# Kernel tuning notes

Measured on AMD Instinct MI355X. Metric: run time of the kernel, lower is better.

The kernel has to match this reference:

```python
import jax, jax.numpy as jnp
import numpy as np

TOP_K = 2

def setup_inputs() -> dict:
    key = jax.random.key(0)
    ks = jax.random.split(key, 5)
    B, S, D, E, R, H = 4, 2048, 1024, 8, 128, 4096
    s = 0.02
    return {
        "hidden_states": jax.random.normal(ks[0], (B, S, D), jnp.float32),
        "w_route": jax.random.normal(ks[1], (E, D, R), jnp.float32) * s,
        "w3": jax.random.normal(ks[2], (E, D, H), jnp.float32) * s,
        "wr2h": jax.random.normal(ks[3], (E, R, H), jnp.float32) * s,
        "wh2d": jax.random.normal(ks[4], (E, H, D), jnp.float32) * s,
    }

def reference(hidden_states, w_route, w3, wr2h, wh2d):
    B, S, D = hidden_states.shape
    E = w_route.shape[0]
    x = hidden_states.reshape(-1, D)                      # [N, D]
    N = x.shape[0]
    # per-expert routing activations (also reused as w1_state inside experts)
    acts = jnp.einsum('nd,edr->ner', x, w_route)          # [N, E, R]
    norms = jnp.linalg.norm(acts, axis=-1)                # [N, E] router logits
    probs = jax.nn.softmax(norms.astype(jnp.float32), axis=-1)
    topw, sel = jax.lax.top_k(probs, TOP_K)               # [N, k]
    topw = topw / topw.sum(axis=-1, keepdims=True)
    topw = topw.astype(x.dtype)
    # dense combine weights: routing weight if expert selected, else 0
    combine = jnp.zeros((N, E), x.dtype).at[jnp.arange(N)[:, None], sel].add(topw)
    out = jnp.zeros_like(x)
    for e in range(E):  # fixed small expert count
        h = (x @ w3[e]) * jax.nn.silu(acts[:, e, :] @ wr2h[e])  # [N, H]
        out = out + (h @ wh2d[e]) * combine[:, e:e + 1]
    final = out.reshape(B, S, D)
    # load balancing loss on the router logits (expert_act_norms)
    mask = jax.nn.one_hot(sel, E, dtype=jnp.float32)      # [N, k, E]
    tokens_per_expert = mask.mean(axis=0)                 # [k, E]
    router_prob_per_expert = probs.mean(axis=0)           # [E]
    bl_loss = jnp.sum(tokens_per_expert * router_prob_per_expert[None, :]) * E
    return final, norms, bl_loss
```

## Files before the change

### kernel.cpp

```cpp
#include <hip/hip_runtime.h>


#define DEV static __device__ __forceinline__

typedef float  f32x4  __attribute__((ext_vector_type(4)));
typedef __bf16 bf16x8 __attribute__((ext_vector_type(8)));

DEV unsigned short f2bf(float f) {
  union { float f; unsigned u; } v; v.f = f;
  unsigned r = v.u + 0x7fffu + ((v.u >> 16) & 1u);
  return (unsigned short)(r >> 16);
}
DEV float bf2f(unsigned short b) {
  union { unsigned u; float f; } v; v.u = ((unsigned)b) << 16;
  return v.f;
}

DEV void gll16(const void* g, void* l) {
  __builtin_amdgcn_global_load_lds(
      (const __attribute__((address_space(1))) unsigned int*)g,
      (__attribute__((address_space(3))) unsigned int*)l, 16, 0, 0);
}

DEV f32x4 mfma16(bf16x8 a, bf16x8 b, f32x4 c) {
  return __builtin_amdgcn_mfma_f32_16x16x32_bf16(a, b, c, 0, 0, 0);
}

DEV int xcd_swz(int bid, int nwg) {
  int q = nwg >> 3;
  return (bid & 7) * q + (bid >> 3);
}

DEV void stage_linear(const unsigned short* base, size_t pitch, int k0,
                      unsigned short* lds, int tid) {
  int wq = tid >> 6, lane = tid & 63;
#pragma unroll
  for (int i = 0; i < 4; ++i) {
    int s = wq * 256 + i * 64 + lane;
    int row = s >> 3, b = s & 7;
    int bb = b ^ (row & 7);
    const unsigned short* g = base + (size_t)row * pitch + (size_t)(k0 + bb * 8);
    gll16(g, lds + (size_t)(wq * 256 + i * 64) * 8);
  }
}

DEV void stage_gather(const unsigned short* base, size_t pitch, size_t colOff,
                      int k0, const int* toks, unsigned short* lds, int tid) {
  int wq = tid >> 6, lane = tid & 63;
#pragma unroll
  for (int i = 0; i < 4; ++i) {
    int s = wq * 256 + i * 64 + lane;
    int row = s >> 3, b = s & 7;
    int bb = b ^ (row & 7);
    const unsigned short* g =
        base + (size_t)toks[row] * pitch + colOff + (size_t)(k0 + bb * 8);
    gll16(g, lds + (size_t)(wq * 256 + i * 64) * 8);
  }
}

DEV bf16x8 frag_read(const unsigned short* lds, int row, int kb) {
  int off = row * 128 + ((kb * 2) ^ ((row & 7) << 4));
  return *(const bf16x8*)((const char*)lds + off);
}

DEV void mfma_block(const unsigned short* A, const unsigned short* B,
                    f32x4 (&acc)[4][4], int wm, int wn, int lg, int lc) {
#pragma unroll
  for (int ks = 0; ks < 2; ++ks) {
    int kb = ks * 32 + lg * 8;
    bf16x8 af[4], bff[4];
#pragma unroll
    for (int i = 0; i < 4; ++i) {
      af[i]  = frag_read(A, wm * 64 + i * 16 + lc, kb);
      bff[i] = frag_read(B, wn * 64 + i * 16 + lc, kb);
    }
#pragma unroll
    for (int mf = 0; mf < 4; ++mf)
#pragma unroll
      for (int nf = 0; nf < 4; ++nf)
        acc[mf][nf] = mfma16(af[mf], bff[nf], acc[mf][nf]);
  }
}


__global__ __launch_bounds__(256) void k_cast_x(const float* __restrict__ x,
    unsigned short* __restrict__ xh, unsigned short* __restrict__ xl) {
  int stride = gridDim.x * blockDim.x;
  for (int i = blockIdx.x * blockDim.x + threadIdx.x; i < 8192 * 1024 / 4;
       i += stride) {
    float4 v = ((const float4*)x)[i];
    ushort4 h, l;
    h.x = f2bf(v.x); l.x = f2bf(v.x - bf2f(h.x));
    h.y = f2bf(v.y); l.y = f2bf(v.y - bf2f(h.y));
    h.z = f2bf(v.z); l.z = f2bf(v.z - bf2f(h.z));
    h.w = f2bf(v.w); l.w = f2bf(v.w - bf2f(h.w));
    ((ushort4*)xh)[i] = h;
    ((ushort4*)xl)[i] = l;
  }
}

__global__ void k_zero(int* cnt, float* probsum) {
  int t = threadIdx.x;
  if (t < 16) cnt[t] = 0;
  if (t < 8)  probsum[t] = 0.f;
}

__global__ __launch_bounds__(256) void k_transp(const float* __restrict__ src,
    unsigned short* __restrict__ dst, int K, int N) {
  int ntn = N >> 6;
  int kt = blockIdx.x / ntn, nt = blockIdx.x % ntn;
  int e = blockIdx.y;
  __shared__ float tl[64][65];
  const float* s = src + (size_t)e * K * N;
  unsigned short* d = dst + (size_t)e * N * K;
  int tid = threadIdx.x;
  int c4 = (tid & 15) * 4, rr = tid >> 4;
#pragma unroll
  for (int p = 0; p < 4; ++p) {
    int row = rr + p * 16;
    float4 v = *(const float4*)(s + (size_t)(kt * 64 + row) * N + nt * 64 + c4);
    tl[row][c4] = v.x; tl[row][c4 + 1] = v.y;
    tl[row][c4 + 2] = v.z; tl[row][c4 + 3] = v.w;
  }
  __syncthreads();
#pragma unroll
  for (int p = 0; p < 4; ++p) {
    int n = rr + p * 16;
    ushort4 o;
    o.x = f2bf(tl[c4 + 0][n]); o.y = f2bf(tl[c4 + 1][n]);
    o.z = f2bf(tl[c4 + 2][n]); o.w = f2bf(tl[c4 + 3][n]);
    *(ushort4*)(d + (size_t)(nt * 64 + n) * K + kt * 64 + c4) = o;
  }
// ... 102 lines not shown
    for (int r = 0; r < 4; ++r) {
      float s = ssq[mf][r];
      s += __shfl_xor(s, 1); s += __shfl_xor(s, 2);
      s += __shfl_xor(s, 4); s += __shfl_xor(s, 8);
      if (lc == 0) ssq_s[wm * 64 + mf * 16 + lg * 4 + r][wn] = s;
    }
  __syncthreads();
  if (tid < 128) {
    float s = ssq_s[tid][0] + ssq_s[tid][1];
    norms_out[(size_t)(mt * 128 + tid) * 8 + e] = sqrtf(s);
  }
}

__global__ __launch_bounds__(256) void k_router(const float* __restrict__ norms,
    float* __restrict__ topw, int* __restrict__ sel,
    int* __restrict__ cnt, float* __restrict__ probsum) {
  __shared__ float ps_s[8];
  __shared__ int cnt_s[16];
  int tid = threadIdx.x;
  if (tid < 8)  ps_s[tid] = 0.f;
  if (tid < 16) cnt_s[tid] = 0;
  __syncthreads();
  int n = blockIdx.x * 256 + tid;
  float p[8], mx = -3.4e38f;
#pragma unroll
  for (int e = 0; e < 8; ++e) { p[e] = norms[(size_t)n * 8 + e]; mx = fmaxf(mx, p[e]); }
  float s = 0.f;
#pragma unroll
  for (int e = 0; e < 8; ++e) { p[e] = __expf(p[e] - mx); s += p[e]; }
  float inv = 1.f / s;
  int i1 = 0; float v1 = p[0];
#pragma unroll
  for (int e = 1; e < 8; ++e) if (p[e] > v1) { v1 = p[e]; i1 = e; }
  int i2 = -1; float v2 = -1.f;
#pragma unroll
  for (int e = 0; e < 8; ++e) if (e != i1 && p[e] > v2) { v2 = p[e]; i2 = e; }
  float wsum = v1 + v2;
  topw[n * 2 + 0] = v1 / wsum;
  topw[n * 2 + 1] = v2 / wsum;
  sel[n * 2 + 0] = i1;
  sel[n * 2 + 1] = i2;
  atomicAdd(&cnt_s[i1], 1);
  atomicAdd(&cnt_s[8 + i2], 1);
#pragma unroll
  for (int e = 0; e < 8; ++e) atomicAdd(&ps_s[e], p[e] * inv);
  __syncthreads();
  if (tid < 8)  atomicAdd(&probsum[tid], ps_s[tid]);
  if (tid < 16) atomicAdd(&cnt[tid], cnt_s[tid]);
}

__global__ void k_plan(const int* __restrict__ cnt, const float* __restrict__ probsum,
                       int* __restrict__ offs, int* __restrict__ fill,
                       int4* __restrict__ tilemap, float* __restrict__ bl_out) {
  int t = 0;
  for (int k = 0; k < 2; ++k) {
    int pos = 0;
    for (int e = 0; e < 8; ++e) {
      int c = cnt[k * 8 + e];
      offs[k * 8 + e] = pos;
      int ntl = (c + 127) >> 7;
      for (int i = 0; i < ntl; ++i) {
        int rr = c - i * 128; if (rr > 128) rr = 128;
        tilemap[t] = make_int4(e, k * 8192 + pos + i * 128, rr, 0);
        ++t;
      }
      pos += c;
    }
  }
  for (; t < 144; ++t) tilemap[t] = make_int4(0, 0, 0, 0);
  for (int i = 0; i < 16; ++i) fill[i] = 0;
  float bl = 0.f;
  for (int e = 0; e < 8; ++e)
    bl += ((float)(cnt[e] + cnt[8 + e]) / 8192.f) * (probsum[e] / 8192.f);
  *bl_out = bl * 8.f;
}

__global__ __launch_bounds__(256) void k_fill(const int* __restrict__ sel,
    const float* __restrict__ topw, const int* __restrict__ offs,
    int* __restrict__ fill, int* __restrict__ list01, float* __restrict__ wlist) {
  int n = blockIdx.x * 256 + threadIdx.x;
#pragma unroll
  for (int k = 0; k < 2; ++k) {
    int e = sel[n * 2 + k];
    int pos = atomicAdd(&fill[k * 8 + e], 1);
    int idx = k * 8192 + offs[k * 8 + e] + pos;
    list01[idx] = n;
    wlist[idx] = topw[n * 2 + k];
  }
}

__global__ __launch_bounds__(256) void k_gemm1(
    const unsigned short* __restrict__ xh, const unsigned short* __restrict__ acts,
    const unsigned short* __restrict__ w3t, const unsigned short* __restrict__ wr2h_t,
    const int* __restrict__ list, const int4* __restrict__ tilemap, int tile_lo,
    int nt, unsigned short* __restrict__ hbuf) {
  __shared__ __align__(16) unsigned short SA[2 * 128 * 64];
  __shared__ __align__(16) unsigned short SB[2 * 128 * 64];
  __shared__ int toks[128];
  int wg = xcd_swz(blockIdx.x, nt * 32);
  int tileIdx = wg >> 5, bn = wg & 31;
  int4 ent = tilemap[tile_lo + tileIdx];
  int e = ent.x, posbase = ent.y, rows = ent.z;
  if (rows == 0) return;
  int tid = threadIdx.x;
  if (tid < 128) {
    int rr = tid < rows ? tid : rows - 1;
    toks[tid] = list[posbase + rr];
  }
  __syncthreads();
  int wq = tid >> 6, lane = tid & 63;
  int wm = wq >> 1, wn = wq & 1, lg = lane >> 4, lc = lane & 15;
  f32x4 acc_a[4][4] = {};
  const unsigned short* bsrc = w3t + ((size_t)e * 4096 + bn * 128) * 1024;
  stage_gather(xh, 1024, 0, 0, toks, SA, tid);
  stage_linear(bsrc, 1024, 0, SB, tid);
  __syncthreads();
  int cur = 0;
  for (int kt = 0; kt < 15; ++kt) {
    int nxt = cur ^ 1;
    stage_gather(xh, 1024, 0, (kt + 1) * 64, toks, SA + nxt * 8192, tid);
    stage_linear(bsrc, 1024, (kt + 1) * 64, SB + nxt * 8192, tid);
    mfma_block(SA + cur * 8192, SB + cur * 8192, acc_a, wm, wn, lg, lc);
    __syncthreads();
    cur = nxt;
  }
  mfma_block(SA + cur * 8192, SB + cur * 8192, acc_a, wm, wn, lg, lc);
  __syncthreads();
  f32x4 acc_s[4][4] = {};
  const unsigned short* b2src = wr2h_t + ((size_t)e * 4096 + bn * 128) * 128;
  stage_gather(acts, 1024, (size_t)e * 128, 0, toks, SA, tid);
  stage_linear(b2src, 128, 0, SB, tid);
  stage_gather(acts, 1024, (size_t)e * 128, 64, toks, SA + 8192, tid);
  stage_linear(b2src, 128, 64, SB + 8192, tid);
  __syncthreads();
  mfma_block(SA, SB, acc_s, wm, wn, lg, lc);
  mfma_block(SA + 8192, SB + 8192, acc_s, wm, wn, lg, lc);
  size_t hrow0 = (size_t)tileIdx * 128;
#pragma unroll
  for (int mf = 0; mf < 4; ++mf)
#pragma unroll
    for (int nf = 0; nf < 4; ++nf)
#pragma unroll
      for (int r = 0; r < 4; ++r) {
        int row = wm * 64 + mf * 16 + lg * 4 + r;
        if (row < rows) {
          int col = wn * 64 + nf * 16 + lc;
          float sv = acc_s[mf][nf][r];
          float hv = acc_a[mf][nf][r] * (sv / (1.f + __expf(-sv)));
          hbuf[(hrow0 + row) * 4096 + (size_t)bn * 128 + col] = f2bf(hv);
        }
      }
}

__global__ __launch_bounds__(256) void k_gemm2(
    const unsigned short* __restrict__ hbuf, const unsigned short* __restrict__ wh2dt,
    const int* __restrict__ list, const float* __restrict__ wlist,
    const int4* __restrict__ tilemap, int tile_lo, int nt,
    float* __restrict__ out) {
  __shared__ __align__(16) unsigned short SA[2 * 128 * 64];
  __shared__ __align__(16) unsigned short SB[2 * 128 * 64];
  __shared__ int toks[128];
  __shared__ float wr_s[128];
  int wg = xcd_swz(blockIdx.x, nt * 8);
  int tileIdx = wg >> 3, bn = wg & 7;
  int4 ent = tilemap[tile_lo + tileIdx];
  int e = ent.x, posbase = ent.y, rows = ent.z;
  if (rows == 0) return;
  int tid = threadIdx.x;
  if (tid < 128) {
    int rr = tid < rows ? tid : rows - 1;
    toks[tid] = list[posbase + rr];
    wr_s[tid] = wlist[posbase + rr];
  }
  __syncthreads();
  int wq = tid >> 6, lane = tid & 63;
  int wm = wq >> 1, wn = wq & 1, lg = lane >> 4, lc = lane & 15;
  f32x4 acc[4][4] = {};
  const unsigned short* asrc = hbuf + (size_t)tileIdx * 128 * 4096;
  const unsigned short* bsrc = wh2dt + ((size_t)e * 1024 + bn * 128) * 4096;
  stage_linear(asrc, 4096, 0, SA, tid);
  stage_linear(bsrc, 4096, 0, SB, tid);
  __syncthreads();
  int cur = 0;
  for (int kt = 0; kt < 63; ++kt) {
    int nxt = cur ^ 1;
    stage_linear(asrc, 4096, (kt + 1) * 64, SA + nxt * 8192, tid);
    stage_linear(bsrc, 4096, (kt + 1) * 64, SB + nxt * 8192, tid);
    mfma_block(SA + cur * 8192, SB + cur * 8192, acc, wm, wn, lg, lc);
    __syncthreads();
    cur = nxt;
  }
  mfma_block(SA + cur * 8192, SB + cur * 8192, acc, wm, wn, lg, lc);
#pragma unroll
  for (int mf = 0; mf < 4; ++mf)
#pragma unroll
    for (int nf = 0; nf < 4; ++nf)
#pragma unroll
      for (int r = 0; r < 4; ++r) {
        int row = wm * 64 + mf * 16 + lg * 4 + r;
        if (row < rows) {
          int col = wn * 64 + nf * 16 + lc;
          float v = acc[mf][nf][r] * wr_s[row];
          atomicAdd(out + (size_t)toks[row] * 1024 + bn * 128 + col, v);
        }
      }
}


extern "C" void kernel_launch(void* const* d_in, const int* in_sizes, int n_in,
                              void* d_out, int out_size, void* d_ws, size_t ws_size,
                              hipStream_t stream) {
  (void)in_sizes; (void)n_in; (void)out_size;
  const float* x      = (const float*)d_in[0];
  const float* wroute = (const float*)d_in[1];
  const float* w3     = (const float*)d_in[2];
  const float* wr2h   = (const float*)d_in[3];
  const float* wh2d   = (const float*)d_in[4];
  float* out = (float*)d_out;

  char* ws = (char*)d_ws;
  size_t off = 0;
  auto carve = [&](size_t bytes) -> void* {
    void* p = ws + off; off += (bytes + 255) & ~(size_t)255; return p;
  };
  unsigned short* xh     = (unsigned short*)carve((size_t)8192 * 1024 * 2);
  unsigned short* xl     = (unsigned short*)carve((size_t)8192 * 1024 * 2);
  unsigned short* wrh_t  = (unsigned short*)carve((size_t)8 * 128 * 1024 * 2);
  unsigned short* wrl_t  = (unsigned short*)carve((size_t)8 * 128 * 1024 * 2);
  unsigned short* w3t    = (unsigned short*)carve((size_t)8 * 4096 * 1024 * 2);
  unsigned short* wr2h_t = (unsigned short*)carve((size_t)8 * 4096 * 128 * 2);
  unsigned short* wh2dt  = (unsigned short*)carve((size_t)8 * 1024 * 4096 * 2);
  unsigned short* acts   = (unsigned short*)carve((size_t)8192 * 1024 * 2);
  int*   list01 = (int*)carve(2 * 8192 * 4);
  float* wlist  = (float*)carve(2 * 8192 * 4);
  int*   sel    = (int*)carve(8192 * 2 * 4);
  float* topw   = (float*)carve(8192 * 2 * 4);
  int*   ctr    = (int*)carve(8192);
  int* cnt = ctr; int* fill = ctr + 16; int* offs = ctr + 32;
  float* probsum = (float*)(ctr + 48);
  int4* tilemap = (int4*)(ctr + 64);

  size_t avail = ws_size > off ? ws_size - off : 0;
  int tpc = 0;
  const int cands[8] = {144, 72, 48, 36, 24, 18, 12, 9};
  for (int i = 0; i < 8; ++i) {
    if ((size_t)cands[i] * 128 * 4096 * 2 <= avail) { tpc = cands[i]; break; }
  }
  if (!tpc) return;
  unsigned short* hbuf = (unsigned short*)(ws + off);

  float* norms_out = out + 8388608;
  float* bl_out    = out + 8454144;

  hipMemsetAsync(out, 0, (size_t)8388608 * 4, stream);
  k_cast_x<<<2048, 256, 0, stream>>>(x, xh, xl);
  k_zero<<<1, 64, 0, stream>>>(cnt, probsum);
  k_transp<<<dim3(16 * 64, 8), 256, 0, stream>>>(w3, w3t, 1024, 4096);
  k_transp<<<dim3(64 * 16, 8), 256, 0, stream>>>(wh2d, wh2dt, 4096, 1024);
  k_transp<<<dim3(2 * 64, 8), 256, 0, stream>>>(wr2h, wr2h_t, 128, 4096);
  k_transp_split<<<dim3(16 * 2, 8), 256, 0, stream>>>(wroute, wrh_t, wrl_t, 1024, 128);
  k_route_gemm<<<dim3(64, 8), 256, 0, stream>>>(xh, xl, wrh_t, wrl_t, acts, norms_out);
  k_router<<<32, 256, 0, stream>>>(norms_out, topw, sel, cnt, probsum);
  k_plan<<<1, 1, 0, stream>>>(cnt, probsum, offs, fill, tilemap, bl_out);
  k_fill<<<32, 256, 0, stream>>>(sel, topw, offs, fill, list01, wlist);

  int nchunk = (144 + tpc - 1) / tpc;
  for (int c = 0; c < nchunk; ++c) {
    int tile_lo = c * tpc;
    int nt = 144 - tile_lo < tpc ? 144 - tile_lo : tpc;
    k_gemm1<<<nt * 32, 256, 0, stream>>>(
        xh, acts, w3t, wr2h_t, list01, tilemap, tile_lo, nt, hbuf);
    k_gemm2<<<nt * 8, 256, 0, stream>>>(
        hbuf, wh2dt, list01, wlist, tilemap, tile_lo, nt, out);
  }
}
```

Before: 889.9 us.

## Enlarge expert GEMM tiles to 256 rows with 512-thread workgroups

Grouped expert GEMMs now use 256-token tiles instead of 128. gemm1 uses 256x128 tiles over 8 waves and prefetches the wr2h stage into the double buffer. gemm2 uses 256x256 tiles, which halves the weight reloads per token and the number of output atomics per element. The planner now emits at most 80 tiles and uses a generalized XCD swizzle for grid sizes not divisible by 8. Larger tiles add more padding waste on partially filled expert tiles, and the bigger LDS footprint (128KB in gemm2) may limit occupancy.

```diff
diff --git a/kernel.cpp b/kernel.cpp
--- a/kernel.cpp
+++ b/kernel.cpp
@@ -26,9 +26,15 @@
   return __builtin_amdgcn_mfma_f32_16x16x32_bf16(a, b, c, 0, 0, 0);
 }
 
-DEV int xcd_swz(int bid, int nwg) {
-  int q = nwg >> 3;
-  return (bid & 7) * q + (bid >> 3);
+DEV int xcd_swz_gen(int bid, int nwg) {
+  int x = bid & 7, o = bid >> 3;
+  int q = nwg >> 3, r = nwg & 7;
+  return (x < r ? x * (q + 1) : r * (q + 1) + (x - r) * q) + o;
+}
+
+DEV bf16x8 frag_read(const unsigned short* lds, int row, int kb) {
+  int off = row * 128 + ((kb * 2) ^ ((row & 7) << 4));
+  return *(const bf16x8*)((const char*)lds + off);
 }
 
 DEV void stage_linear(const unsigned short* base, size_t pitch, int k0,
@@ -44,23 +50,44 @@
   }
 }
 
-DEV void stage_gather(const unsigned short* base, size_t pitch, size_t colOff,
-                      int k0, const int* toks, unsigned short* lds, int tid) {
+DEV void stage_l256(const unsigned short* base, size_t pitch, int k0,
+                    unsigned short* lds, int tid) {
   int wq = tid >> 6, lane = tid & 63;
 #pragma unroll
   for (int i = 0; i < 4; ++i) {
-    int s = wq * 256 + i * 64 + lane;
+    int sb = wq * 256 + i * 64;
+    int s = sb + lane;
     int row = s >> 3, b = s & 7;
     int bb = b ^ (row & 7);
-    const unsigned short* g =
-        base + (size_t)toks[row] * pitch + colOff + (size_t)(k0 + bb * 8);
-    gll16(g, lds + (size_t)(wq * 256 + i * 64) * 8);
-  }
-}
-
-DEV bf16x8 frag_read(const unsigned short* lds, int row, int kb) {
-  int off = row * 128 + ((kb * 2) ^ ((row & 7) << 4));
-  return *(const bf16x8*)((const char*)lds + off);
+    gll16(base + (size_t)row * pitch + (size_t)(k0 + bb * 8),
+          lds + (size_t)sb * 8);
+  }
+}
+DEV void stage_g256(const unsigned short* base, size_t pitch, size_t colOff,
+                    int k0, const int* toks, unsigned short* lds, int tid) {
+  int wq = tid >> 6, lane = tid & 63;
+#pragma unroll
+  for (int i = 0; i < 4; ++i) {
+    int sb = wq * 256 + i * 64;
+    int s = sb + lane;
+    int row = s >> 3, b = s & 7;
+    int bb = b ^ (row & 7);
+    gll16(base + (size_t)toks[row] * pitch + colOff + (size_t)(k0 + bb * 8),
+          lds + (size_t)sb * 8);
+  }
+}
+DEV void stage_l128(const unsigned short* base, size_t pitch, int k0,
+                    unsigned short* lds, int tid) {
+  int wq = tid >> 6, lane = tid & 63;
+#pragma unroll
+  for (int i = 0; i < 2; ++i) {
+    int sb = wq * 128 + i * 64;
+    int s = sb + lane;
+    int row = s >> 3, b = s & 7;
+    int bb = b ^ (row & 7);
+    gll16(base + (size_t)row * pitch + (size_t)(k0 + bb * 8),
+          lds + (size_t)sb * 8);
+  }
 }
 
 DEV void mfma_block(const unsigned short* A, const unsigned short* B,
@@ -78,6 +105,40 @@
     for (int mf = 0; mf < 4; ++mf)
 #pragma unroll
       for (int nf = 0; nf < 4; ++nf)
+        acc[mf][nf] = mfma16(af[mf], bff[nf], acc[mf][nf]);
+  }
+}
+DEV void mfma256x256(const unsigned short* A, const unsigned short* B,
+                     f32x4 (&acc)[8][4], int wm, int wn, int lg, int lc) {
+#pragma unroll
+  for (int ks = 0; ks < 2; ++ks) {
+    int kb = ks * 32 + lg * 8;
+    bf16x8 af[8], bff[4];
+#pragma unroll
+    for (int i = 0; i < 8; ++i) af[i] = frag_read(A, wm * 128 + i * 16 + lc, kb);
+#pragma unroll
+    for (int i = 0; i < 4; ++i) bff[i] = frag_read(B, wn * 64 + i * 16 + lc, kb);
+#pragma unroll
+    for (int mf = 0; mf < 8; ++mf)
+#pragma unroll
+      for (int nf = 0; nf < 4; ++nf)
+        acc[mf][nf] = mfma16(af[mf], bff[nf], acc[mf][nf]);
+  }
+}
+DEV void mfma256x128(const unsigned short* A, const unsigned short* B,
+                     f32x4 (&acc)[8][2], int wm, int wn, int lg, int lc) {
+#pragma unroll
+  for (int ks = 0; ks < 2; ++ks) {
+    int kb = ks * 32 + lg * 8;
+    bf16x8 af[8], bff[2];
+#pragma unroll
+    for (int i = 0; i < 8; ++i) af[i] = frag_read(A, wm * 128 + i * 16 + lc, kb);
+#pragma unroll
+    for (int i = 0; i < 2; ++i) bff[i] = frag_read(B, wn * 32 + i * 16 + lc, kb);
+#pragma unroll
+    for (int mf = 0; mf < 8; ++mf)
+#pragma unroll
+      for (int nf = 0; nf < 2; ++nf)
         acc[mf][nf] = mfma16(af[mf], bff[nf], acc[mf][nf]);
   }
 }
@@ -292,16 +353,16 @@
     for (int e = 0; e < 8; ++e) {
       int c = cnt[k * 8 + e];
       offs[k * 8 + e] = pos;
-      int ntl = (c + 127) >> 7;
+      int ntl = (c + 255) >> 8;
       for (int i = 0; i < ntl; ++i) {
-        int rr = c - i * 128; if (rr > 128) rr = 128;
-        tilemap[t] = make_int4(e, k * 8192 + pos + i * 128, rr, 0);
+        int rr = c - i * 256; if (rr > 256) rr = 256;
+        tilemap[t] = make_int4(e, k * 8192 + pos + i * 256, rr, 0);
         ++t;
       }
       pos += c;
     }
   }
-  for (; t < 144; ++t) tilemap[t] = make_int4(0, 0, 0, 0);
+  for (; t < 80; ++t) tilemap[t] = make_int4(0, 0, 0, 0);
   for (int i = 0; i < 16; ++i) fill[i] = 0;
   float bl = 0.f;
   for (int e = 0; e < 8; ++e)
@@ -323,62 +384,62 @@
   }
 }
 
-__global__ __launch_bounds__(256) void k_gemm1(
+__global__ __launch_bounds__(512, 2) void k_gemm1(
     const unsigned short* __restrict__ xh, const unsigned short* __restrict__ acts,
     const unsigned short* __restrict__ w3t, const unsigned short* __restrict__ wr2h_t,
     const int* __restrict__ list, const int4* __restrict__ tilemap, int tile_lo,
     int nt, unsigned short* __restrict__ hbuf) {
-  __shared__ __align__(16) unsigned short SA[2 * 128 * 64];
-  __shared__ __align__(16) unsigned short SB[2 * 128 * 64];
-  __shared__ int toks[128];
-  int wg = xcd_swz(blockIdx.x, nt * 32);
-  int tileIdx = wg >> 5, bn = wg & 31;
-  int4 ent = tilemap[tile_lo + tileIdx];
+  __shared__ __align__(16) unsigned short SA[2][256 * 64];
+  __shared__ __align__(16) unsigned short SB[2][128 * 64];
+  __shared__ int toks[256];
+  int wg = xcd_swz_gen((int)blockIdx.x, nt * 32);
+  int tloc = wg >> 5, bn = wg & 31;
+  int4 ent = tilemap[tile_lo + tloc];
   int e = ent.x, posbase = ent.y, rows = ent.z;
   if (rows == 0) return;
   int tid = threadIdx.x;
-  if (tid < 128) {
+  if (tid < 256) {
     int rr = tid < rows ? tid : rows - 1;
     toks[tid] = list[posbase + rr];
   }
   __syncthreads();
   int wq = tid >> 6, lane = tid & 63;
-  int wm = wq >> 1, wn = wq & 1, lg = lane >> 4, lc = lane & 15;
-  f32x4 acc_a[4][4] = {};
-  const unsigned short* bsrc = w3t + ((size_t)e * 4096 + bn * 128) * 1024;
-  stage_gather(xh, 1024, 0, 0, toks, SA, tid);
-  stage_linear(bsrc, 1024, 0, SB, tid);
+  int wm = wq >> 2, wn = wq & 3, lg = lane >> 4, lc = lane & 15;
+  f32x4 acc_a[8][2] = {}, acc_s[8][2] = {};
+  const unsigned short* bsrc  = w3t + ((size_t)e * 4096 + bn * 128) * 1024;
+  const unsigned short* b2src = wr2h_t + ((size_t)e * 4096 + bn * 128) * 128;
+  stage_g256(xh, 1024, 0, 0, toks, SA[0], tid);
+  stage_l128(bsrc, 1024, 0, SB[0], tid);
   __syncthreads();
   int cur = 0;
   for (int kt = 0; kt < 15; ++kt) {
-    int nxt = cur ^ 1;
-    stage_gather(xh, 1024, 0, (kt + 1) * 64, toks, SA + nxt * 8192, tid);
-    stage_linear(bsrc, 1024, (kt + 1) * 64, SB + nxt * 8192, tid);
-    mfma_block(SA + cur * 8192, SB + cur * 8192, acc_a, wm, wn, lg, lc);
+    stage_g256(xh, 1024, 0, (kt + 1) * 64, toks, SA[cur ^ 1], tid);
+    stage_l128(bsrc, 1024, (kt + 1) * 64, SB[cur ^ 1], tid);
+    mfma256x128(SA[cur], SB[cur], acc_a, wm, wn, lg, lc);
     __syncthreads();
-    cur = nxt;
-  }
-  mfma_block(SA + cur * 8192, SB + cur * 8192, acc_a, wm, wn, lg, lc);
-  __syncthreads();
-  f32x4 acc_s[4][4] = {};
-  const unsigned short* b2src = wr2h_t + ((size_t)e * 4096 + bn * 128) * 128;
-  stage_gather(acts, 1024, (size_t)e * 128, 0, toks, SA, tid);
-  stage_linear(b2src, 128, 0, SB, tid);
-  stage_gather(acts, 1024, (size_t)e * 128, 64, toks, SA + 8192, tid);
-  stage_linear(b2src, 128, 64, SB + 8192, tid);
-  __syncthreads();
-  mfma_block(SA, SB, acc_s, wm, wn, lg, lc);
-  mfma_block(SA + 8192, SB + 8192, acc_s, wm, wn, lg, lc);
-  size_t hrow0 = (size_t)tileIdx * 128;
-#pragma unroll
-  for (int mf = 0; mf < 4; ++mf)
-#pragma unroll
-    for (int nf = 0; nf < 4; ++nf)
+    cur ^= 1;
+  }
+  stage_g256(acts, 1024, (size_t)e * 128, 0, toks, SA[cur ^ 1], tid);
+  stage_l128(b2src, 128, 0, SB[cur ^ 1], tid);
+  mfma256x128(SA[cur], SB[cur], acc_a, wm, wn, lg, lc);
+  __syncthreads();
+  cur ^= 1;
+  stage_g256(acts, 1024, (size_t)e * 128, 64, toks, SA[cur ^ 1], tid);
+  stage_l128(b2src, 128, 64, SB[cur ^ 1], tid);
+  mfma256x128(SA[cur], SB[cur], acc_s, wm, wn, lg, lc);
+  __syncthreads();
+  cur ^= 1;
+  mfma256x128(SA[cur], SB[cur], acc_s, wm, wn, lg, lc);
+  size_t hrow0 = (size_t)tloc * 256;
+#pragma unroll
+  for (int mf = 0; mf < 8; ++mf)
+#pragma unroll
+    for (int nf = 0; nf < 2; ++nf)
 #pragma unroll
       for (int r = 0; r < 4; ++r) {
-        int row = wm * 64 + mf * 16 + lg * 4 + r;
+        int row = wm * 128 + mf * 16 + lg * 4 + r;
         if (row < rows) {
-          int col = wn * 64 + nf * 16 + lc;
+          int col = wn * 32 + nf * 16 + lc;
           float sv = acc_s[mf][nf][r];
           float hv = acc_a[mf][nf][r] * (sv / (1.f + __expf(-sv)));
           hbuf[(hrow0 + row) * 4096 + (size_t)bn * 128 + col] = f2bf(hv);
@@ -386,56 +447,56 @@
       }
 }
 
-__global__ __launch_bounds__(256) void k_gemm2(
+__global__ __launch_bounds__(512, 2) void k_gemm2(
     const unsigned short* __restrict__ hbuf, const unsigned short* __restrict__ wh2dt,
     const int* __restrict__ list, const float* __restrict__ wlist,
     const int4* __restrict__ tilemap, int tile_lo, int nt,
     float* __restrict__ out) {
-  __shared__ __align__(16) unsigned short SA[2 * 128 * 64];
-  __shared__ __align__(16) unsigned short SB[2 * 128 * 64];
-  __shared__ int toks[128];
-  __shared__ float wr_s[128];
-  int wg = xcd_swz(blockIdx.x, nt * 8);
-  int tileIdx = wg >> 3, bn = wg & 7;
-  int4 ent = tilemap[tile_lo + tileIdx];
+  __shared__ __align__(16) unsigned short SA[2][256 * 64];
+  __shared__ __align__(16) unsigned short SB[2][256 * 64];
+  __shared__ int toks[256];
+  __shared__ float wr_s[256];
+  int wg = xcd_swz_gen((int)blockIdx.x, nt * 4);
+  int tloc = wg >> 2, bn = wg & 3;
+  int4 ent = tilemap[tile_lo + tloc];
   int e = ent.x, posbase = ent.y, rows = ent.z;
   if (rows == 0) return;
   int tid = threadIdx.x;
-  if (tid < 128) {
+  if (tid < 256) {
     int rr = tid < rows ? tid : rows - 1;
-    toks[tid] = list[posbase + rr];
+    int t = list[posbase + rr];
+    toks[tid] = t;
     wr_s[tid] = wlist[posbase + rr];
   }
   __syncthreads();
   int wq = tid >> 6, lane = tid & 63;
-  int wm = wq >> 1, wn = wq & 1, lg = lane >> 4, lc = lane & 15;
-  f32x4 acc[4][4] = {};
-  const unsigned short* asrc = hbuf + (size_t)tileIdx * 128 * 4096;
-  const unsigned short* bsrc = wh2dt + ((size_t)e * 1024 + bn * 128) * 4096;
-  stage_linear(asrc, 4096, 0, SA, tid);
-  stage_linear(bsrc, 4096, 0, SB, tid);
+  int wm = wq >> 2, wn = wq & 3, lg = lane >> 4, lc = lane & 15;
+  f32x4 acc[8][4] = {};
+  const unsigned short* asrc = hbuf + (size_t)tloc * 256 * 4096;
+  const unsigned short* bsrc = wh2dt + ((size_t)e * 1024 + bn * 256) * 4096;
+  stage_l256(asrc, 4096, 0, SA[0], tid);
+  stage_l256(bsrc, 4096, 0, SB[0], tid);
   __syncthreads();
   int cur = 0;
   for (int kt = 0; kt < 63; ++kt) {
-    int nxt = cur ^ 1;
-    stage_linear(asrc, 4096, (kt + 1) * 64, SA + nxt * 8192, tid);
-    stage_linear(bsrc, 4096, (kt + 1) * 64, SB + nxt * 8192, tid);
-    mfma_block(SA + cur * 8192, SB + cur * 8192, acc, wm, wn, lg, lc);
+    stage_l256(asrc, 4096, (kt + 1) * 64, SA[cur ^ 1], tid);
+    stage_l256(bsrc, 4096, (kt + 1) * 64, SB[cur ^ 1], tid);
+    mfma256x256(SA[cur], SB[cur], acc, wm, wn, lg, lc);
     __syncthreads();
-    cur = nxt;
-  }
-  mfma_block(SA + cur * 8192, SB + cur * 8192, acc, wm, wn, lg, lc);
-#pragma unroll
-  for (int mf = 0; mf < 4; ++mf)
+    cur ^= 1;
+  }
+  mfma256x256(SA[cur], SB[cur], acc, wm, wn, lg, lc);
+#pragma unroll
+  for (int mf = 0; mf < 8; ++mf)
 #pragma unroll
     for (int nf = 0; nf < 4; ++nf)
 #pragma unroll
       for (int r = 0; r < 4; ++r) {
-        int row = wm * 64 + mf * 16 + lg * 4 + r;
+        int row = wm * 128 + mf * 16 + lg * 4 + r;
         if (row < rows) {
           int col = wn * 64 + nf * 16 + lc;
           float v = acc[mf][nf][r] * wr_s[row];
-          atomicAdd(out + (size_t)toks[row] * 1024 + bn * 128 + col, v);
+          atomicAdd(out + (size_t)toks[row] * 1024 + bn * 256 + col, v);
         }
       }
 }
@@ -476,9 +537,9 @@
 
   size_t avail = ws_size > off ? ws_size - off : 0;
   int tpc = 0;
-  const int cands[8] = {144, 72, 48, 36, 24, 18, 12, 9};
-  for (int i = 0; i < 8; ++i) {
-    if ((size_t)cands[i] * 128 * 4096 * 2 <= avail) { tpc = cands[i]; break; }
+  const int cands[4] = {80, 40, 20, 10};
+  for (int i = 0; i < 4; ++i) {
+    if ((size_t)cands[i] * 256 * 4096 * 2 <= avail) { tpc = cands[i]; break; }
   }
   if (!tpc) return;
   unsigned short* hbuf = (unsigned short*)(ws + off);
@@ -498,13 +559,13 @@
   k_plan<<<1, 1, 0, stream>>>(cnt, probsum, offs, fill, tilemap, bl_out);
   k_fill<<<32, 256, 0, stream>>>(sel, topw, offs, fill, list01, wlist);
 
-  int nchunk = (144 + tpc - 1) / tpc;
+  int nchunk = (80 + tpc - 1) / tpc;
   for (int c = 0; c < nchunk; ++c) {
     int tile_lo = c * tpc;
-    int nt = 144 - tile_lo < tpc ? 144 - tile_lo : tpc;
-    k_gemm1<<<nt * 32, 256, 0, stream>>>(
+    int nt = 80 - tile_lo < tpc ? 80 - tile_lo : tpc;
+    k_gemm1<<<nt * 32, 512, 0, stream>>>(
         xh, acts, w3t, wr2h_t, list01, tilemap, tile_lo, nt, hbuf);
-    k_gemm2<<<nt * 8, 256, 0, stream>>>(
+    k_gemm2<<<nt * 4, 512, 0, stream>>>(
         hbuf, wh2dt, list01, wlist, tilemap, tile_lo, nt, out);
   }
 }
```

Result: slower. 955.0 us (+7.3%).

## Enlarge MoE GEMM tiles to 256, add triple-buffered K=32 pipeline with 512 threads

Applied to the files above, without the earlier changes.

Routing tiles grow from 128 to 256 tokens, and the two expert GEMMs now run with 8 waves per block. GEMM1 uses 256x128 tiles and GEMM2 uses 128x256 tiles, with a triple-buffered LDS pipeline over K=32 steps. The pipeline is driven by explicit vmcnt waits, raw barriers and MFMA priority boosts, and the SiLU-gate GEMM is folded into the same pipeline. The aim is to raise weight reuse per token tile and hide global-to-LDS latency better, at the cost of more padding waste on partially filled 256-row tiles and a more fragile hand-written schedule.

```diff
diff --git a/kernel.cpp b/kernel.cpp
--- a/kernel.cpp
+++ b/kernel.cpp
@@ -5,6 +5,10 @@
 
 typedef float  f32x4  __attribute__((ext_vector_type(4)));
 typedef __bf16 bf16x8 __attribute__((ext_vector_type(8)));
+
+#define VMCNT_(n) asm volatile("s_waitcnt vmcnt(" #n ")" ::: "memory")
+#define VMCNT(n) VMCNT_(n)
+#define SBAR()   asm volatile("s_barrier" ::: "memory")
 
 DEV unsigned short f2bf(float f) {
   union { float f; unsigned u; } v; v.f = f;
@@ -26,11 +30,26 @@
   return __builtin_amdgcn_mfma_f32_16x16x32_bf16(a, b, c, 0, 0, 0);
 }
 
-DEV int xcd_swz(int bid, int nwg) {
-  int q = nwg >> 3;
-  return (bid & 7) * q + (bid >> 3);
-}
-
+DEV int xcd_swz_gen(int bid, int nwg) {
+  int x = bid & 7, o = bid >> 3;
+  int q = nwg >> 3, r = nwg & 7;
+  return (x < r ? x * (q + 1) : r * (q + 1) + (x - r) * q) + o;
+}
+
+DEV int swz_slot(int s) {
+  int p = s >> 3, w0 = (s & 7) ^ (p & 7);
+  return (((p << 1) | (w0 >> 2)) << 2) | (w0 & 3);
+}
+DEV bf16x8 frag_read32(const unsigned short* lds, int row, int lg) {
+  int p = row >> 1;
+  int off = p * 128 + (((((row & 1) << 2) | lg) ^ (p & 7)) << 4);
+  return *(const bf16x8*)((const char*)lds + off);
+}
+
+DEV bf16x8 frag_read(const unsigned short* lds, int row, int kb) {
+  int off = row * 128 + ((kb * 2) ^ ((row & 7) << 4));
+  return *(const bf16x8*)((const char*)lds + off);
+}
 DEV void stage_linear(const unsigned short* base, size_t pitch, int k0,
                       unsigned short* lds, int tid) {
   int wq = tid >> 6, lane = tid & 63;
@@ -43,26 +62,6 @@
     gll16(g, lds + (size_t)(wq * 256 + i * 64) * 8);
   }
 }
-
-DEV void stage_gather(const unsigned short* base, size_t pitch, size_t colOff,
-                      int k0, const int* toks, unsigned short* lds, int tid) {
-  int wq = tid >> 6, lane = tid & 63;
-#pragma unroll
-  for (int i = 0; i < 4; ++i) {
-    int s = wq * 256 + i * 64 + lane;
-    int row = s >> 3, b = s & 7;
-    int bb = b ^ (row & 7);
-    const unsigned short* g =
-        base + (size_t)toks[row] * pitch + colOff + (size_t)(k0 + bb * 8);
-    gll16(g, lds + (size_t)(wq * 256 + i * 64) * 8);
-  }
-}
-
-DEV bf16x8 frag_read(const unsigned short* lds, int row, int kb) {
-  int off = row * 128 + ((kb * 2) ^ ((row & 7) << 4));
-  return *(const bf16x8*)((const char*)lds + off);
-}
-
 DEV void mfma_block(const unsigned short* A, const unsigned short* B,
                     f32x4 (&acc)[4][4], int wm, int wn, int lg, int lc) {
 #pragma unroll
@@ -286,22 +285,32 @@
 __global__ void k_plan(const int* __restrict__ cnt, const float* __restrict__ probsum,
                        int* __restrict__ offs, int* __restrict__ fill,
                        int4* __restrict__ tilemap, float* __restrict__ bl_out) {
+  int4* map256 = tilemap;
+  int4* map128 = tilemap + 80;
   int t = 0;
   for (int k = 0; k < 2; ++k) {
     int pos = 0;
     for (int e = 0; e < 8; ++e) {
       int c = cnt[k * 8 + e];
       offs[k * 8 + e] = pos;
-      int ntl = (c + 127) >> 7;
+      int ntl = (c + 255) >> 8;
       for (int i = 0; i < ntl; ++i) {
-        int rr = c - i * 128; if (rr > 128) rr = 128;
-        tilemap[t] = make_int4(e, k * 8192 + pos + i * 128, rr, 0);
+        int rr = c - i * 256; if (rr > 256) rr = 256;
+        map256[t] = make_int4(e, k * 8192 + pos + i * 256, rr, 0);
         ++t;
       }
       pos += c;
     }
   }
-  for (; t < 144; ++t) tilemap[t] = make_int4(0, 0, 0, 0);
+  for (; t < 80; ++t) map256[t] = make_int4(0, 0, 0, 0);
+  for (int i = 0; i < 80; ++i) {
+    int4 m = map256[i];
+    for (int h = 0; h < 2; ++h) {
+      int r = m.z - h * 128;
+      if (r < 0) r = 0; if (r > 128) r = 128;
+      map128[i * 2 + h] = make_int4(m.x, m.y + h * 128, r, i * 256 + h * 128);
+    }
+  }
   for (int i = 0; i < 16; ++i) fill[i] = 0;
   float bl = 0.f;
   for (int e = 0; e < 8; ++e)
@@ -323,53 +332,83 @@
   }
 }
 
-__global__ __launch_bounds__(256) void k_gemm1(
+__global__ __launch_bounds__(512, 2) void k_gemm1(
     const unsigned short* __restrict__ xh, const unsigned short* __restrict__ acts,
     const unsigned short* __restrict__ w3t, const unsigned short* __restrict__ wr2h_t,
     const int* __restrict__ list, const int4* __restrict__ tilemap, int tile_lo,
     int nt, unsigned short* __restrict__ hbuf) {
-  __shared__ __align__(16) unsigned short SA[2 * 128 * 64];
-  __shared__ __align__(16) unsigned short SB[2 * 128 * 64];
-  __shared__ int toks[128];
-  int wg = xcd_swz(blockIdx.x, nt * 32);
-  int tileIdx = wg >> 5, bn = wg & 31;
-  int4 ent = tilemap[tile_lo + tileIdx];
+  __shared__ __align__(16) unsigned short SA[3][256 * 32];
+  __shared__ __align__(16) unsigned short SB[3][128 * 32];
+  __shared__ int toks[256];
+  int wg = xcd_swz_gen((int)blockIdx.x, nt * 32);
+  int tloc = wg >> 5, bn = wg & 31;
+  int4 ent = tilemap[tile_lo + tloc];
   int e = ent.x, posbase = ent.y, rows = ent.z;
   if (rows == 0) return;
   int tid = threadIdx.x;
-  if (tid < 128) {
+  if (tid < 256) {
     int rr = tid < rows ? tid : rows - 1;
     toks[tid] = list[posbase + rr];
   }
   __syncthreads();
   int wq = tid >> 6, lane = tid & 63;
   int wm = wq >> 1, wn = wq & 1, lg = lane >> 4, lc = lane & 15;
-  f32x4 acc_a[4][4] = {};
-  const unsigned short* bsrc = w3t + ((size_t)e * 4096 + bn * 128) * 1024;
-  stage_gather(xh, 1024, 0, 0, toks, SA, tid);
-  stage_linear(bsrc, 1024, 0, SB, tid);
-  __syncthreads();
-  int cur = 0;
-  for (int kt = 0; kt < 15; ++kt) {
-    int nxt = cur ^ 1;
-    stage_gather(xh, 1024, 0, (kt + 1) * 64, toks, SA + nxt * 8192, tid);
-    stage_linear(bsrc, 1024, (kt + 1) * 64, SB + nxt * 8192, tid);
-    mfma_block(SA + cur * 8192, SB + cur * 8192, acc_a, wm, wn, lg, lc);
-    __syncthreads();
-    cur = nxt;
-  }
-  mfma_block(SA + cur * 8192, SB + cur * 8192, acc_a, wm, wn, lg, lc);
-  __syncthreads();
-  f32x4 acc_s[4][4] = {};
-  const unsigned short* b2src = wr2h_t + ((size_t)e * 4096 + bn * 128) * 128;
-  stage_gather(acts, 1024, (size_t)e * 128, 0, toks, SA, tid);
-  stage_linear(b2src, 128, 0, SB, tid);
-  stage_gather(acts, 1024, (size_t)e * 128, 64, toks, SA + 8192, tid);
-  stage_linear(b2src, 128, 64, SB + 8192, tid);
-  __syncthreads();
-  mfma_block(SA, SB, acc_s, wm, wn, lg, lc);
-  mfma_block(SA + 8192, SB + 8192, acc_s, wm, wn, lg, lc);
-  size_t hrow0 = (size_t)tileIdx * 128;
+  int sA0 = wq * 128 + lane, sA1 = sA0 + 64;
+  int sB0 = wq * 64 + lane;
+  int vA0 = swz_slot(sA0), vA1 = swz_slot(sA1), vB0 = swz_slot(sB0);
+  const unsigned short* gA0 = xh + (size_t)toks[vA0 >> 2] * 1024 + (vA0 & 3) * 8;
+  const unsigned short* gA1 = xh + (size_t)toks[vA1 >> 2] * 1024 + (vA1 & 3) * 8;
+  const unsigned short* qA0 = acts + (size_t)toks[vA0 >> 2] * 1024 + e * 128 + (vA0 & 3) * 8;
+  const unsigned short* qA1 = acts + (size_t)toks[vA1 >> 2] * 1024 + e * 128 + (vA1 & 3) * 8;
+  const unsigned short* gB0 =
+      w3t + ((size_t)e * 4096 + bn * 128 + (vB0 >> 2)) * 1024 + (vB0 & 3) * 8;
+  const unsigned short* qB0 =
+      wr2h_t + ((size_t)e * 4096 + bn * 128 + (vB0 >> 2)) * 128 + (vB0 & 3) * 8;
+  f32x4 acc_a[4][4] = {}, acc_s[4][4] = {};
+
+  auto stage1 = [&](int tt, int bs) {
+    unsigned short* dA0 = &SA[bs][(size_t)sA0 * 8];
+    unsigned short* dA1 = &SA[bs][(size_t)sA1 * 8];
+    unsigned short* dB0 = &SB[bs][(size_t)sB0 * 8];
+    if (tt < 32) {
+      int k0 = tt * 32;
+      gll16(gA0 + k0, dA0); gll16(gA1 + k0, dA1); gll16(gB0 + k0, dB0);
+    } else {
+      int k0 = (tt - 32) * 32;
+      gll16(qA0 + k0, dA0); gll16(qA1 + k0, dA1); gll16(qB0 + k0, dB0);
+    }
+  };
+
+  stage1(0, 0); stage1(1, 1);
+  int cur = 0, bs = 2;
+
+#define G1_TILE(VMN, DO_STAGE, STT, ACC)                                     \
+  {                                                                          \
+    VMCNT(VMN); SBAR();                                                      \
+    bf16x8 af[4], bf[4];                                                     \
+    _Pragma("unroll") for (int i = 0; i < 4; ++i)                            \
+      af[i] = frag_read32(&SA[cur][0], wm * 64 + i * 16 + lc, lg);           \
+    _Pragma("unroll") for (int i = 0; i < 4; ++i)                            \
+      bf[i] = frag_read32(&SB[cur][0], wn * 64 + i * 16 + lc, lg);           \
+    if (DO_STAGE) stage1(STT, bs);                                           \
+    SBAR();                                                                  \
+    __builtin_amdgcn_s_setprio(1);                                           \
+    _Pragma("unroll") for (int mf = 0; mf < 4; ++mf)                         \
+      _Pragma("unroll") for (int nf = 0; nf < 4; ++nf)                       \
+        ACC[mf][nf] = mfma16(af[mf], bf[nf], ACC[mf][nf]);                   \
+    __builtin_amdgcn_s_setprio(0);                                           \
+    cur = cur == 2 ? 0 : cur + 1;                                            \
+    bs  = bs  == 2 ? 0 : bs  + 1;                                            \
+  }
+
+  for (int t = 0; t < 32; ++t) G1_TILE(3, true, t + 2, acc_a);
+  G1_TILE(3, true, 34, acc_s);
+  G1_TILE(3, true, 35, acc_s);
+  G1_TILE(3, false, 0, acc_s);
+  G1_TILE(0, false, 0, acc_s);
+#undef G1_TILE
+
+  size_t hrow0 = (size_t)tloc * 256;
 #pragma unroll
   for (int mf = 0; mf < 4; ++mf)
 #pragma unroll
@@ -386,20 +425,21 @@
       }
 }
 
-__global__ __launch_bounds__(256) void k_gemm2(
+__global__ __launch_bounds__(512, 2) void k_gemm2(
     const unsigned short* __restrict__ hbuf, const unsigned short* __restrict__ wh2dt,
     const int* __restrict__ list, const float* __restrict__ wlist,
-    const int4* __restrict__ tilemap, int tile_lo, int nt,
+    const int4* __restrict__ map128, int tile_lo, int nt,
     float* __restrict__ out) {
-  __shared__ __align__(16) unsigned short SA[2 * 128 * 64];
-  __shared__ __align__(16) unsigned short SB[2 * 128 * 64];
+  __shared__ __align__(16) unsigned short SA[3][128 * 32];
+  __shared__ __align__(16) unsigned short SB[3][256 * 32];
   __shared__ int toks[128];
   __shared__ float wr_s[128];
-  int wg = xcd_swz(blockIdx.x, nt * 8);
-  int tileIdx = wg >> 3, bn = wg & 7;
-  int4 ent = tilemap[tile_lo + tileIdx];
+  int wg = xcd_swz_gen((int)blockIdx.x, nt * 8);
+  int tloc = wg >> 2, bn = wg & 3;
+  int4 ent = map128[tile_lo * 2 + tloc];
   int e = ent.x, posbase = ent.y, rows = ent.z;
   if (rows == 0) return;
+  int hb = ent.w - tile_lo * 256;
   int tid = threadIdx.x;
   if (tid < 128) {
     int rr = tid < rows ? tid : rows - 1;
@@ -408,23 +448,51 @@
   }
   __syncthreads();
   int wq = tid >> 6, lane = tid & 63;
-  int wm = wq >> 1, wn = wq & 1, lg = lane >> 4, lc = lane & 15;
+  int wm = wq >> 2, wn = wq & 3, lg = lane >> 4, lc = lane & 15;
+  int sA0 = wq * 64 + lane;
+  int sB0 = wq * 128 + lane, sB1 = sB0 + 64;
+  int vA0 = swz_slot(sA0), vB0 = swz_slot(sB0), vB1 = swz_slot(sB1);
+  const unsigned short* gA0 = hbuf + (size_t)(hb + (vA0 >> 2)) * 4096 + (vA0 & 3) * 8;
+  const unsigned short* gB0 =
+      wh2dt + ((size_t)e * 1024 + bn * 256 + (vB0 >> 2)) * 4096 + (vB0 & 3) * 8;
+  const unsigned short* gB1 =
+      wh2dt + ((size_t)e * 1024 + bn * 256 + (vB1 >> 2)) * 4096 + (vB1 & 3) * 8;
   f32x4 acc[4][4] = {};
-  const unsigned short* asrc = hbuf + (size_t)tileIdx * 128 * 4096;
-  const unsigned short* bsrc = wh2dt + ((size_t)e * 1024 + bn * 128) * 4096;
-  stage_linear(asrc, 4096, 0, SA, tid);
-  stage_linear(bsrc, 4096, 0, SB, tid);
-  __syncthreads();
-  int cur = 0;
-  for (int kt = 0; kt < 63; ++kt) {
-    int nxt = cur ^ 1;
-    stage_linear(asrc, 4096, (kt + 1) * 64, SA + nxt * 8192, tid);
-    stage_linear(bsrc, 4096, (kt + 1) * 64, SB + nxt * 8192, tid);
-    mfma_block(SA + cur * 8192, SB + cur * 8192, acc, wm, wn, lg, lc);
-    __syncthreads();
-    cur = nxt;
-  }
-  mfma_block(SA + cur * 8192, SB + cur * 8192, acc, wm, wn, lg, lc);
+
+  auto stage2 = [&](int tt, int bs) {
+    int k0 = tt * 32;
+    gll16(gA0 + k0, &SA[bs][(size_t)sA0 * 8]);
+    gll16(gB0 + k0, &SB[bs][(size_t)sB0 * 8]);
+    gll16(gB1 + k0, &SB[bs][(size_t)sB1 * 8]);
+  };
+
+  stage2(0, 0); stage2(1, 1);
+  int cur = 0, bs = 2;
+
+#define G2_TILE(VMN, DO_STAGE, STT)                                          \
+  {                                                                          \
+    VMCNT(VMN); SBAR();                                                      \
+    bf16x8 af[4], bf[4];                                                     \
+    _Pragma("unroll") for (int i = 0; i < 4; ++i)                            \
+      af[i] = frag_read32(&SA[cur][0], wm * 64 + i * 16 + lc, lg);           \
+    _Pragma("unroll") for (int i = 0; i < 4; ++i)                            \
+      bf[i] = frag_read32(&SB[cur][0], wn * 64 + i * 16 + lc, lg);           \
+    if (DO_STAGE) stage2(STT, bs);                                           \
+    SBAR();                                                                  \
+    __builtin_amdgcn_s_setprio(1);                                           \
+    _Pragma("unroll") for (int mf = 0; mf < 4; ++mf)                         \
+      _Pragma("unroll") for (int nf = 0; nf < 4; ++nf)                       \
+        acc[mf][nf] = mfma16(af[mf], bf[nf], acc[mf][nf]);                   \
+    __builtin_amdgcn_s_setprio(0);                                           \
+    cur = cur == 2 ? 0 : cur + 1;                                            \
+    bs  = bs  == 2 ? 0 : bs  + 1;                                            \
+  }
+
+  for (int t = 0; t < 126; ++t) G2_TILE(3, true, t + 2);
+  G2_TILE(3, false, 0);
+  G2_TILE(0, false, 0);
+#undef G2_TILE
+
 #pragma unroll
   for (int mf = 0; mf < 4; ++mf)
 #pragma unroll
@@ -435,7 +503,7 @@
         if (row < rows) {
           int col = wn * 64 + nf * 16 + lc;
           float v = acc[mf][nf][r] * wr_s[row];
-          atomicAdd(out + (size_t)toks[row] * 1024 + bn * 128 + col, v);
+          atomicAdd(out + (size_t)toks[row] * 1024 + bn * 256 + col, v);
         }
       }
 }
@@ -476,9 +544,9 @@
 
   size_t avail = ws_size > off ? ws_size - off : 0;
   int tpc = 0;
-  const int cands[8] = {144, 72, 48, 36, 24, 18, 12, 9};
-  for (int i = 0; i < 8; ++i) {
-    if ((size_t)cands[i] * 128 * 4096 * 2 <= avail) { tpc = cands[i]; break; }
+  const int cands[4] = {80, 40, 20, 10};
+  for (int i = 0; i < 4; ++i) {
+    if ((size_t)cands[i] * 256 * 4096 * 2 <= avail) { tpc = cands[i]; break; }
   }
   if (!tpc) return;
   unsigned short* hbuf = (unsigned short*)(ws + off);
@@ -498,13 +566,13 @@
   k_plan<<<1, 1, 0, stream>>>(cnt, probsum, offs, fill, tilemap, bl_out);
   k_fill<<<32, 256, 0, stream>>>(sel, topw, offs, fill, list01, wlist);
 
-  int nchunk = (144 + tpc - 1) / tpc;
+  int nchunk = (80 + tpc - 1) / tpc;
   for (int c = 0; c < nchunk; ++c) {
     int tile_lo = c * tpc;
-    int nt = 144 - tile_lo < tpc ? 144 - tile_lo : tpc;
-    k_gemm1<<<nt * 32, 256, 0, stream>>>(
+    int nt = 80 - tile_lo < tpc ? 80 - tile_lo : tpc;
+    k_gemm1<<<nt * 32, 512, 0, stream>>>(
         xh, acts, w3t, wr2h_t, list01, tilemap, tile_lo, nt, hbuf);
-    k_gemm2<<<nt * 8, 256, 0, stream>>>(
-        hbuf, wh2dt, list01, wlist, tilemap, tile_lo, nt, out);
-  }
-}
+    k_gemm2<<<nt * 8, 512, 0, stream>>>(
+        hbuf, wh2dt, list01, wlist, tilemap + 80, tile_lo, nt, out);
+  }
+}
```

New measurement: 859.1 us. 3.5% less time.

## Split gemm2 along K, drop LDS double buffering, generalize XCD swizzle

Applied to the files above, without the earlier changes.

Replaces the double-buffered LDS pipelines in both expert GEMM kernels with single-buffered load/sync/compute/sync loops, halving shared memory per block. The down-projection GEMM is split into two K halves, each accumulated into the output with atomics, doubling its grid. The tile map is padded from 144 to 160 entries and the XCD swizzle handles workgroup counts that are not multiples of 8. The smaller LDS footprint and larger gemm2 grid are meant to raise occupancy and parallelism, at the cost of losing load/compute overlap within a block and adding more atomic traffic.

```diff
diff --git a/kernel.cpp b/kernel.cpp
--- a/kernel.cpp
+++ b/kernel.cpp
@@ -26,11 +26,16 @@
   return __builtin_amdgcn_mfma_f32_16x16x32_bf16(a, b, c, 0, 0, 0);
 }
 
-DEV int xcd_swz(int bid, int nwg) {
-  int q = nwg >> 3;
-  return (bid & 7) * q + (bid >> 3);
-}
-
+DEV int xcd_swz_gen(int bid, int nwg) {
+  int x = bid & 7, o = bid >> 3;
+  int q = nwg >> 3, r = nwg & 7;
+  return (x < r ? x * (q + 1) : r * (q + 1) + (x - r) * q) + o;
+}
+
+DEV bf16x8 frag_read(const unsigned short* lds, int row, int kb) {
+  int off = row * 128 + ((kb * 2) ^ ((row & 7) << 4));
+  return *(const bf16x8*)((const char*)lds + off);
+}
 DEV void stage_linear(const unsigned short* base, size_t pitch, int k0,
                       unsigned short* lds, int tid) {
   int wq = tid >> 6, lane = tid & 63;
@@ -43,7 +48,6 @@
     gll16(g, lds + (size_t)(wq * 256 + i * 64) * 8);
   }
 }
-
 DEV void stage_gather(const unsigned short* base, size_t pitch, size_t colOff,
                       int k0, const int* toks, unsigned short* lds, int tid) {
   int wq = tid >> 6, lane = tid & 63;
@@ -57,12 +61,6 @@
     gll16(g, lds + (size_t)(wq * 256 + i * 64) * 8);
   }
 }
-
-DEV bf16x8 frag_read(const unsigned short* lds, int row, int kb) {
-  int off = row * 128 + ((kb * 2) ^ ((row & 7) << 4));
-  return *(const bf16x8*)((const char*)lds + off);
-}
-
 DEV void mfma_block(const unsigned short* A, const unsigned short* B,
                     f32x4 (&acc)[4][4], int wm, int wn, int lg, int lc) {
 #pragma unroll
@@ -301,7 +299,7 @@
       pos += c;
     }
   }
-  for (; t < 144; ++t) tilemap[t] = make_int4(0, 0, 0, 0);
+  for (; t < 160; ++t) tilemap[t] = make_int4(0, 0, 0, 0);
   for (int i = 0; i < 16; ++i) fill[i] = 0;
   float bl = 0.f;
   for (int e = 0; e < 8; ++e)
@@ -328,12 +326,11 @@
     const unsigned short* __restrict__ w3t, const unsigned short* __restrict__ wr2h_t,
     const int* __restrict__ list, const int4* __restrict__ tilemap, int tile_lo,
     int nt, unsigned short* __restrict__ hbuf) {
-  __shared__ __align__(16) unsigned short SA[2 * 128 * 64];
-  __shared__ __align__(16) unsigned short SB[2 * 128 * 64];
+  __shared__ __align__(16) unsigned short A[128 * 64], B[128 * 64];
   __shared__ int toks[128];
-  int wg = xcd_swz(blockIdx.x, nt * 32);
-  int tileIdx = wg >> 5, bn = wg & 31;
-  int4 ent = tilemap[tile_lo + tileIdx];
+  int wg = xcd_swz_gen((int)blockIdx.x, nt * 32);
+  int tloc = wg >> 5, bn = wg & 31;
+  int4 ent = tilemap[tile_lo + tloc];
   int e = ent.x, posbase = ent.y, rows = ent.z;
   if (rows == 0) return;
   int tid = threadIdx.x;
@@ -346,30 +343,25 @@
   int wm = wq >> 1, wn = wq & 1, lg = lane >> 4, lc = lane & 15;
   f32x4 acc_a[4][4] = {};
   const unsigned short* bsrc = w3t + ((size_t)e * 4096 + bn * 128) * 1024;
-  stage_gather(xh, 1024, 0, 0, toks, SA, tid);
-  stage_linear(bsrc, 1024, 0, SB, tid);
-  __syncthreads();
-  int cur = 0;
-  for (int kt = 0; kt < 15; ++kt) {
-    int nxt = cur ^ 1;
-    stage_gather(xh, 1024, 0, (kt + 1) * 64, toks, SA + nxt * 8192, tid);
-    stage_linear(bsrc, 1024, (kt + 1) * 64, SB + nxt * 8192, tid);
-    mfma_block(SA + cur * 8192, SB + cur * 8192, acc_a, wm, wn, lg, lc);
-    __syncthreads();
-    cur = nxt;
-  }
-  mfma_block(SA + cur * 8192, SB + cur * 8192, acc_a, wm, wn, lg, lc);
-  __syncthreads();
+  for (int kt = 0; kt < 16; ++kt) {
+    int k0 = kt * 64;
+    stage_gather(xh, 1024, 0, k0, toks, A, tid);
+    stage_linear(bsrc, 1024, k0, B, tid);
+    __syncthreads();
+    mfma_block(A, B, acc_a, wm, wn, lg, lc);
+    __syncthreads();
+  }
   f32x4 acc_s[4][4] = {};
   const unsigned short* b2src = wr2h_t + ((size_t)e * 4096 + bn * 128) * 128;
-  stage_gather(acts, 1024, (size_t)e * 128, 0, toks, SA, tid);
-  stage_linear(b2src, 128, 0, SB, tid);
-  stage_gather(acts, 1024, (size_t)e * 128, 64, toks, SA + 8192, tid);
-  stage_linear(b2src, 128, 64, SB + 8192, tid);
-  __syncthreads();
-  mfma_block(SA, SB, acc_s, wm, wn, lg, lc);
-  mfma_block(SA + 8192, SB + 8192, acc_s, wm, wn, lg, lc);
-  size_t hrow0 = (size_t)tileIdx * 128;
+  for (int kt = 0; kt < 2; ++kt) {
+    int k0 = kt * 64;
+    stage_gather(acts, 1024, (size_t)e * 128, k0, toks, A, tid);
+    stage_linear(b2src, 128, k0, B, tid);
+    __syncthreads();
+    mfma_block(A, B, acc_s, wm, wn, lg, lc);
+    __syncthreads();
+  }
+  size_t hrow0 = (size_t)tloc * 128;
 #pragma unroll
   for (int mf = 0; mf < 4; ++mf)
 #pragma unroll
@@ -391,13 +383,12 @@
     const int* __restrict__ list, const float* __restrict__ wlist,
     const int4* __restrict__ tilemap, int tile_lo, int nt,
     float* __restrict__ out) {
-  __shared__ __align__(16) unsigned short SA[2 * 128 * 64];
-  __shared__ __align__(16) unsigned short SB[2 * 128 * 64];
+  __shared__ __align__(16) unsigned short A[128 * 64], B[128 * 64];
   __shared__ int toks[128];
   __shared__ float wr_s[128];
-  int wg = xcd_swz(blockIdx.x, nt * 8);
-  int tileIdx = wg >> 3, bn = wg & 7;
-  int4 ent = tilemap[tile_lo + tileIdx];
+  int wg = xcd_swz_gen((int)blockIdx.x, nt * 16);
+  int tloc = wg >> 4, bn = (wg >> 1) & 7, ks = wg & 1;
+  int4 ent = tilemap[tile_lo + tloc];
   int e = ent.x, posbase = ent.y, rows = ent.z;
   if (rows == 0) return;
   int tid = threadIdx.x;
@@ -410,21 +401,17 @@
   int wq = tid >> 6, lane = tid & 63;
   int wm = wq >> 1, wn = wq & 1, lg = lane >> 4, lc = lane & 15;
   f32x4 acc[4][4] = {};
-  const unsigned short* asrc = hbuf + (size_t)tileIdx * 128 * 4096;
+  const unsigned short* asrc = hbuf + (size_t)tloc * 128 * 4096;
   const unsigned short* bsrc = wh2dt + ((size_t)e * 1024 + bn * 128) * 4096;
-  stage_linear(asrc, 4096, 0, SA, tid);
-  stage_linear(bsrc, 4096, 0, SB, tid);
-  __syncthreads();
-  int cur = 0;
-  for (int kt = 0; kt < 63; ++kt) {
-    int nxt = cur ^ 1;
-    stage_linear(asrc, 4096, (kt + 1) * 64, SA + nxt * 8192, tid);
-    stage_linear(bsrc, 4096, (kt + 1) * 64, SB + nxt * 8192, tid);
-    mfma_block(SA + cur * 8192, SB + cur * 8192, acc, wm, wn, lg, lc);
-    __syncthreads();
-    cur = nxt;
-  }
-  mfma_block(SA + cur * 8192, SB + cur * 8192, acc, wm, wn, lg, lc);
+  int kbase = ks * 2048;
+  for (int kt = 0; kt < 32; ++kt) {
+    int k0 = kbase + kt * 64;
+    stage_linear(asrc, 4096, k0, A, tid);
+    stage_linear(bsrc, 4096, k0, B, tid);
+    __syncthreads();
+    mfma_block(A, B, acc, wm, wn, lg, lc);
+    __syncthreads();
+  }
 #pragma unroll
   for (int mf = 0; mf < 4; ++mf)
 #pragma unroll
@@ -476,8 +463,8 @@
 
   size_t avail = ws_size > off ? ws_size - off : 0;
   int tpc = 0;
-  const int cands[8] = {144, 72, 48, 36, 24, 18, 12, 9};
-  for (int i = 0; i < 8; ++i) {
+  const int cands[4] = {160, 80, 40, 20};
+  for (int i = 0; i < 4; ++i) {
     if ((size_t)cands[i] * 128 * 4096 * 2 <= avail) { tpc = cands[i]; break; }
   }
   if (!tpc) return;
@@ -498,13 +485,13 @@
   k_plan<<<1, 1, 0, stream>>>(cnt, probsum, offs, fill, tilemap, bl_out);
   k_fill<<<32, 256, 0, stream>>>(sel, topw, offs, fill, list01, wlist);
 
-  int nchunk = (144 + tpc - 1) / tpc;
+  int nchunk = (160 + tpc - 1) / tpc;
   for (int c = 0; c < nchunk; ++c) {
     int tile_lo = c * tpc;
-    int nt = 144 - tile_lo < tpc ? 144 - tile_lo : tpc;
+    int nt = 160 - tile_lo < tpc ? 160 - tile_lo : tpc;
     k_gemm1<<<nt * 32, 256, 0, stream>>>(
         xh, acts, w3t, wr2h_t, list01, tilemap, tile_lo, nt, hbuf);
-    k_gemm2<<<nt * 8, 256, 0, stream>>>(
+    k_gemm2<<<nt * 16, 256, 0, stream>>>(
         hbuf, wh2dt, list01, wlist, tilemap, tile_lo, nt, out);
   }
 }
```

Measured after the change: 841.5 us. 5.4% less time.
